# Kernel tuning notes

Measured on AMD Instinct MI355X. Metric: run time of the kernel, lower is better.

## Reference

```python
import jax, jax.numpy as jnp
import numpy as np
from jax import lax

EPS = 1e-5
TAU = 2.0
THR = 1.0

@jax.custom_vjp
def spike_fn(x):
    # torch.heaviside(x, 1.0): 1 where x >= 0, else 0
    return (x >= 0).astype(x.dtype)

def _spike_fwd(x):
    return spike_fn(x), x

def _spike_bwd(x, g):
    alpha = 4.0
    s = jax.nn.sigmoid(alpha * x)
    return (g * (1.0 - s) * s * alpha,)

spike_fn.defvjp(_spike_fwd, _spike_bwd)

def lif(x):
    # sequential membrane recurrence over dim 0 (time)
    def step(v, xt):
        v = v + (xt - v) / TAU
        s = spike_fn(v - THR)
        v = (1.0 - lax.stop_gradient(s)) * v
        return v, s
    _, spikes = lax.scan(step, jnp.zeros_like(x[0]), x)
    return spikes

def bn(x, p):
    # eval-mode BatchNorm2d; p = [weight, bias, mean, var], each [C]
    w, b, m, v = p
    inv = w / jnp.sqrt(v + EPS)
    return (x - m[None, :, None, None]) * inv[None, :, None, None] + b[None, :, None, None]

def bn_and_pad(x, p):
    # BN then pad 1 pixel on all sides with the BN-of-zero value
    w, b, m, v = p
    y = bn(x, p)
    pad_val = b - m * w / jnp.sqrt(v + EPS)  # [C]
    y = jnp.pad(y, ((0, 0), (0, 0), (1, 1), (1, 1)))
    pv = pad_val[None, :, None]  # broadcasts over batch and spatial
    y = y.at[:, :, 0, :].set(pv)
    y = y.at[:, :, -1, :].set(pv)
    y = y.at[:, :, :, 0].set(pv)
    y = y.at[:, :, :, -1].set(pv)
    return y

def branch(x, w1, dw, pw, bn3):
    # RepConv: 1x1 -> BNAndPad(1) -> depthwise3x3(valid) -> 1x1 -> BN, then outer BN
    C = x.shape[1]
    y = jnp.einsum('oc,bchw->bohw', w1, x)
    y = bn_and_pad(y, bn3[0])
    y = lax.conv_general_dilated(y, dw[:, None, :, :], (1, 1), 'VALID',
                                 dimension_numbers=('NCHW', 'OIHW', 'NCHW'),
                                 feature_group_count=C)
    y = jnp.einsum('oc,bchw->bohw', pw, y)
    y = bn(y, bn3[1])
    y = bn(y, bn3[2])
    return y

def _to_heads(t, B, N, h, d):
    # [B,C,H,W] -> [B,h,N,d]
    return t.reshape(B, h * d, N).transpose(0, 2, 1).reshape(B, N, h, d).transpose(0, 2, 1, 3)

def forward(x, q_w1, q_dw, q_pw, q_bn, k_w1, k_dw, k_pw, k_bn,
            v_w1, v_dw, v_pw, v_bn, p_w1, p_dw, p_pw, p_bn,
            num_heads=8):
    B, C, H, W = x.shape
    N = H * W
    h = num_heads
    d = C // h
    scale = float(d) ** -0.5

    xs = lif(x)
    q = lif(branch(xs, q_w1, q_dw, q_pw, q_bn))
    k = lif(branch(xs, k_w1, k_dw, k_pw, k_bn))
    v = lif(branch(xs, v_w1, v_dw, v_pw, v_bn))

    q = _to_heads(q, B, N, h, d)
    k = _to_heads(k, B, N, h, d)
    v = _to_heads(v, B, N, h, d)

    kv = jnp.einsum('bhnd,bhne->bhde', k, v)          # [B,h,d,d]
    o = jnp.einsum('bhnd,bhde->bhne', q, kv) * scale  # [B,h,N,d]
    o = o.transpose(0, 1, 3, 2).reshape(B, C, N)       # [B,C,N]
    o = lif(o)
    o = o.reshape(B, C, H, W)
    o = branch(o, p_w1, p_dw, p_pw, p_bn)
    return o.reshape(B, C, H, W)

def setup_inputs() -> dict:
    key = jax.random.key(0)
    ks = jax.random.split(key, 20)
    B, C, H, W = 8, 256, 64, 64
    s1 = 1.0 / np.sqrt(C)

    def make_bn(k):
        k1, k2, k3, k4 = jax.random.split(k, 4)
        w = 1.0 + 0.1 * jax.random.normal(k1, (3, C), jnp.float32)
        b = 0.1 * jax.random.normal(k2, (3, C), jnp.float32)
        m = 0.1 * jax.random.normal(k3, (3, C), jnp.float32)
        var = jax.random.uniform(k4, (3, C), jnp.float32, 0.5, 1.5)
        return jnp.stack([w, b, m, var], axis=1)  # [3,4,C]

    inp = {'x': jax.random.normal(ks[0], (B, C, H, W), jnp.float32)}
    for i, p in enumerate(['q', 'k', 'v', 'p']):
        kk = jax.random.split(ks[1 + i], 4)
        inp[p + '_w1'] = jax.random.normal(kk[0], (C, C), jnp.float32) * s1
        inp[p + '_dw'] = jax.random.normal(kk[1], (C, 3, 3), jnp.float32) * 0.3
        inp[p + '_pw'] = jax.random.normal(kk[2], (C, C), jnp.float32) * s1
        inp[p + '_bn'] = make_bn(kk[3])
    return inp

def reference(x, q_w1, q_dw, q_pw, q_bn, k_w1, k_dw, k_pw, k_bn,
              v_w1, v_dw, v_pw, v_bn, p_w1, p_dw, p_pw, p_bn):
    return forward(x, q_w1, q_dw, q_pw, q_bn, k_w1, k_dw, k_pw, k_bn,
                   v_w1, v_dw, v_pw, v_bn, p_w1, p_dw, p_pw, p_bn)
```

## Files before the change

kernel.cpp:

```cpp
#include <hip/hip_runtime.h>
#include <hip/hip_bf16.h>
#include <math.h>

#define T_ 8
#define C_ 256
#define N_ 4096
#define CN_ (C_ * N_)
#define EPSB 1e-5f

typedef unsigned long long u64;
typedef unsigned int u32;
typedef short bf16x8 __attribute__((ext_vector_type(8)));
typedef short bf16x4 __attribute__((ext_vector_type(4)));
typedef float f32x4 __attribute__((ext_vector_type(4)));

static __device__ __forceinline__ unsigned short f2bf(float f) {
    __hip_bfloat16 h = __float2bfloat16(f);
    return *(unsigned short*)&h;
}
static __device__ __forceinline__ float bf2f(unsigned short u) {
    u32 x = (u32)u << 16;
    return *(float*)&x;
}

typedef const __attribute__((address_space(1))) unsigned int ga_u32;
typedef __attribute__((address_space(3))) unsigned int la_u32;
static __device__ __forceinline__ void gl_lds16(const unsigned short* g,
                                                unsigned short* l_) {
    __builtin_amdgcn_global_load_lds((ga_u32*)g, (la_u32*)l_, 16, 0, 0);
}

#define DRAIN_BAR() asm volatile("s_waitcnt vmcnt(0)\ns_barrier" ::: "memory")


__global__ __launch_bounds__(256) void lif_x_frag(const float* __restrict__ X,
                                                  unsigned short* __restrict__ ST) {
    int n = blockIdx.x * 256 + threadIdx.x;
    int c0 = blockIdx.y * 8;
    int k32 = c0 >> 5, quad = (c0 >> 3) & 3;
    size_t base = (size_t)c0 * N_ + n;
    size_t pos = ((size_t)((n >> 4) * 8 + k32)) * 512 +
                 (size_t)((quad * 16 + (n & 15)) * 8);
    float v[8];
#pragma unroll
    for (int j = 0; j < 8; j++) v[j] = 0.f;
#pragma unroll
    for (int t = 0; t < T_; t++) {
        bf16x8 bs;
#pragma unroll
        for (int j = 0; j < 8; j++) {
            float xt = X[(size_t)t * CN_ + base + (size_t)j * N_];
            float vv = v[j] + (xt - v[j]) / 2.0f;
            int s = (vv - 1.0f >= 0.f) ? 1 : 0;
            bs[j] = s ? (short)0x3F80 : (short)0;
            v[j] = s ? 0.f : vv;
        }
        *(bf16x8*)&ST[(size_t)t * CN_ + pos] = bs;
    }
}

struct LArgs {
    const float* F[3];
    unsigned char* sq;
    u64* kbp;
    u64* vbp;
};
__global__ __launch_bounds__(256) void lif3(LArgs a) {
    int br = blockIdx.y;
    int idx = blockIdx.x * 256 + threadIdx.x;
    const float* X = a.F[br];
    int lane = threadIdx.x & 63;
    u64* BP = (br == 1) ? a.kbp : a.vbp;
    float v = 0.f;
#pragma unroll
    for (int t = 0; t < T_; t++) {
        float xt = X[(size_t)t * CN_ + idx];
        v = v + (xt - v) / 2.0f;
        int s = (v - 1.0f >= 0.f) ? 1 : 0;
        if (br == 0) {
            a.sq[(size_t)t * CN_ + idx] = (unsigned char)s;
        } else {
            u64 mask = __ballot(s);
            if (lane == 0) BP[((size_t)t * CN_ + idx) >> 6] = mask;
        }
        if (s) v = 0.f;
    }
}

struct WPtrs { const float* w[8]; };
__global__ __launch_bounds__(256) void split_w(WPtrs p, unsigned short* __restrict__ out) {
    int mat = blockIdx.y;
    int idx = blockIdx.x * 256 + threadIdx.x;
    int m = idx >> 8, k = idx & 255;
    float w = p.w[mat][idx];
    unsigned short h1 = f2bf(w);
    float f1 = bf2f(h1);
    unsigned short h2 = f2bf(w - f1);
    unsigned short h3 = f2bf(w - f1 - bf2f(h2));
    int lane = ((k >> 3) & 3) * 16 + (m & 15);
    size_t pos = ((size_t)(((m >> 4) * 8 + (k >> 5)) * 64 + lane)) * 8 + (k & 7);
    size_t base = (size_t)mat * 3 * 65536;
    out[base + pos] = h1;
    out[base + 65536 + pos] = h2;
    out[base + 2 * 65536 + pos] = h3;
}

static __device__ __forceinline__ void dw_body(const float* __restrict__ Yt,
                                               const float* __restrict__ dw,
                                               const float* __restrict__ bnp,
                                               unsigned short* __restrict__ Bh,
                                               unsigned short* __restrict__ Bl,
                                               int y0, int cg, int tid) {
    int c0 = cg * 8;
    __shared__ float L[8][10][68];
    __shared__ float invs[8], bs_[8], ms_[8], pads_[8];

    if (tid < 8) {
        int c = c0 + tid;
        float w = bnp[c], b = bnp[256 + c], m = bnp[512 + c], var = bnp[768 + c];
        float sq = sqrtf(var + EPSB);
        invs[tid] = w / sq;
        bs_[tid] = b;
        ms_[tid] = m;
        pads_[tid] = b - (m * w) / sq;
    }
    __syncthreads();

    for (int i = tid; i < 8 * 10 * 66; i += 256) {
        int c = i / 660;
        int rem = i - c * 660;
        int row = rem / 66, col = rem - row * 66;
        int gy = y0 - 1 + row, gx = col - 1;
        float val;
        if (gy < 0 || gy > 63 || gx < 0 || gx > 63) val = pads_[c];
        else val = (Yt[(size_t)(c0 + c) * N_ + gy * 64 + gx] - ms_[c]) * invs[c] + bs_[c];
        L[c][row][col] = val;
    }
    __syncthreads();

    int x = tid & 63, ry = tid >> 6;
#pragma unroll
    for (int h = 0; h < 2; h++) {
        int r = ry + 4 * h;
        int n = (y0 + r) * 64 + x;

        bf16x8 hi, lo;
#pragma unroll
        for (int j = 0; j < 8; j++) {
            const float* dwc = dw + (c0 + j) * 9;
            float a = 0.f;
#pragma unroll
            for (int dy = 0; dy < 3; dy++)
#pragma unroll
                for (int dx = 0; dx < 3; dx++)
                    a += dwc[dy * 3 + dx] * L[j][r + dy][x + dx];
            unsigned short hh = f2bf(a);
            hi[j] = (short)hh;
            lo[j] = (short)f2bf(a - bf2f(hh));
        }
        size_t pos = ((size_t)((n >> 4) * 8 + (cg >> 2))) * 512 +
                     (size_t)(((cg & 3) * 16 + (n & 15)) * 8);
        *(bf16x8*)&Bh[pos] = hi;
        *(bf16x8*)&Bl[pos] = lo;
    }
}

__global__ __launch_bounds__(256) void dw_bn_split(const float* __restrict__ Yin,
                                                   const float* __restrict__ dw,
                                                   const float* __restrict__ bnp,
                                                   unsigned short* __restrict__ BhT,
                                                   unsigned short* __restrict__ BlT) {
    int t = blockIdx.z;
    dw_body(Yin + (size_t)t * CN_, dw, bnp,
            BhT + (size_t)t * CN_, BlT + (size_t)t * CN_,
            blockIdx.x * 8, blockIdx.y, threadIdx.x);
}

struct DArgs {
    const float* F[3];
    const float* dw[3];
    const float* bn[3];
    unsigned short* Ph[3];
    unsigned short* Pl[3];
};
__global__ __launch_bounds__(256) void dw3(DArgs a) {
    int br = blockIdx.z >> 3, t = blockIdx.z & 7;
    dw_body(a.F[br] + (size_t)t * CN_, a.dw[br], a.bn[br],
            a.Ph[br] + (size_t)t * CN_, a.Pl[br] + (size_t)t * CN_,
            blockIdx.x * 8, blockIdx.y, threadIdx.x);
}

static __device__ __forceinline__ void gemm_s_core(const unsigned short* __restrict__ Wsp,
                                                   const unsigned short* __restrict__ Bt,
                                                   float* __restrict__ Yt,
                                                   int bx, int by, int tid) {
    int l = tid & 63, wave = tid >> 6;
    int wm = wave >> 1, wn = wave & 1;
    int lcol = l & 15, quad = l >> 4;

    __shared__ unsigned short As[2][24][512];
    __shared__ unsigned short Bs[2][8][512];

    f32x4 acc[4][4];
#pragma unroll
    for (int i = 0; i < 4; i++)
#pragma unroll
        for (int j = 0; j < 4; j++) acc[i][j] = (f32x4){0.f, 0.f, 0.f, 0.f};

    const unsigned short* src[8];
    unsigned short* d0[8];
    unsigned short* d1[8];
#pragma unroll
    for (int i = 0; i < 8; i++) {
        int tau = wave * 8 + i;
        if (tau < 24) {
            int s = tau >> 3, mtg = tau & 7;
            src[i] = &Wsp[(size_t)s * 65536 + ((size_t)((by * 8 + mtg) * 8)) * 512 + l * 8];
            d0[i] = &As[0][tau][0];
            d1[i] = &As[1][tau][0];
        } else {
            int nt = tau - 24;
            src[i] = &Bt[((size_t)((bx * 8 + nt) * 8)) * 512 + l * 8];
            d0[i] = &Bs[0][nt][0];
            d1[i] = &Bs[1][nt][0];
        }
    }

    auto stg0 = [&]() {
#pragma unroll
        for (int i = 0; i < 8; i++) { gl_lds16(src[i], d0[i]); src[i] += 512; }
    };
    auto stg1 = [&]() {
#pragma unroll
        for (int i = 0; i < 8; i++) { gl_lds16(src[i], d1[i]); src[i] += 512; }
    };
    auto compute = [&](const unsigned short (*Asp)[512],
                       const unsigned short (*Bsp)[512]) {
        bf16x8 bfr[4];
#pragma unroll
        for (int nt = 0; nt < 4; nt++)
            bfr[nt] = *(const bf16x8*)&Bsp[wn * 4 + nt][l * 8];
#pragma unroll
        for (int s = 0; s < 3; s++)
#pragma unroll
            for (int mt = 0; mt < 4; mt++) {
                bf16x8 afr = *(const bf16x8*)&Asp[s * 8 + wm * 4 + mt][l * 8];
#pragma unroll
                for (int nt = 0; nt < 4; nt++)
                    acc[mt][nt] = __builtin_amdgcn_mfma_f32_16x16x32_bf16(
                        afr, bfr[nt], acc[mt][nt], 0, 0, 0);
            }
    };

    stg0();
    DRAIN_BAR();

    for (int kk = 0; kk < 8; kk += 2) {
        stg1();
        compute(As[0], Bs[0]);
        DRAIN_BAR();
        if (kk < 6) stg0();
        compute(As[1], Bs[1]);
        DRAIN_BAR();
    }

    int m0 = by * 128, n0 = bx * 128;
#pragma unroll
    for (int mt = 0; mt < 4; mt++)
#pragma unroll
        for (int i = 0; i < 4; i++) {
            int row = m0 + wm * 64 + mt * 16 + quad * 4 + i;
            float* yr = &Yt[(size_t)row * N_ + n0 + wn * 64 + lcol];
#pragma unroll
            for (int nt = 0; nt < 4; nt++) yr[nt * 16] = acc[mt][nt][i];
        }
}

static __device__ __forceinline__ void gemm_f_core(const unsigned short* __restrict__ Wsp,
                                                   const unsigned short* __restrict__ Bht,
                                                   const unsigned short* __restrict__ Blt,
                                                   float* __restrict__ Yt,
                                                   const float* __restrict__ bnp,
                                                   int bx, int by, int tid) {
    int l = tid & 63, wave = tid >> 6;
    int wm = wave >> 1, wn = wave & 1;
    int lcol = l & 15, quad = l >> 4;

    __shared__ unsigned short As[2][24][512];
    __shared__ unsigned short Bhs[2][8][512];
    __shared__ unsigned short Bls[2][8][512];

    f32x4 acc[4][4];
#pragma unroll
    for (int i = 0; i < 4; i++)
#pragma unroll
        for (int j = 0; j < 4; j++) acc[i][j] = (f32x4){0.f, 0.f, 0.f, 0.f};

    const unsigned short* src[10];
    unsigned short* d0[10];
    unsigned short* d1[10];
#pragma unroll
    for (int i = 0; i < 10; i++) {
        int tau = wave * 10 + i;
        if (tau < 24) {
            int s = tau >> 3, mtg = tau & 7;
            src[i] = &Wsp[(size_t)s * 65536 + ((size_t)((by * 8 + mtg) * 8)) * 512 + l * 8];
            d0[i] = &As[0][tau][0];
            d1[i] = &As[1][tau][0];
        } else if (tau < 32) {
            int nt = tau - 24;
            src[i] = &Bht[((size_t)((bx * 8 + nt) * 8)) * 512 + l * 8];
            d0[i] = &Bhs[0][nt][0];
            d1[i] = &Bhs[1][nt][0];
        } else {
            int nt = tau - 32;
            src[i] = &Blt[((size_t)((bx * 8 + nt) * 8)) * 512 + l * 8];
            d0[i] = &Bls[0][nt][0];
            d1[i] = &Bls[1][nt][0];
        }
    }

    auto stg0 = [&]() {
#pragma unroll
        for (int i = 0; i < 10; i++) { gl_lds16(src[i], d0[i]); src[i] += 512; }
    };
    auto stg1 = [&]() {
#pragma unroll
        for (int i = 0; i < 10; i++) { gl_lds16(src[i], d1[i]); src[i] += 512; }
    };
    auto compute = [&](const unsigned short (*Asp)[512],
                       const unsigned short (*Bhp)[512],
                       const unsigned short (*Blp)[512]) {
        bf16x8 bh[4], bl[4];
#pragma unroll
        for (int nt = 0; nt < 4; nt++) {
            bh[nt] = *(const bf16x8*)&Bhp[wn * 4 + nt][l * 8];
            bl[nt] = *(const bf16x8*)&Blp[wn * 4 + nt][l * 8];
        }
#pragma unroll
        for (int s = 0; s < 3; s++)
#pragma unroll
            for (int mt = 0; mt < 4; mt++) {
                bf16x8 afr = *(const bf16x8*)&Asp[s * 8 + wm * 4 + mt][l * 8];
#pragma unroll
                for (int nt = 0; nt < 4; nt++)
                    acc[mt][nt] = __builtin_amdgcn_mfma_f32_16x16x32_bf16(
                        afr, bh[nt], acc[mt][nt], 0, 0, 0);
                if (s < 2) {
#pragma unroll
                    for (int nt = 0; nt < 4; nt++)
                        acc[mt][nt] = __builtin_amdgcn_mfma_f32_16x16x32_bf16(
                            afr, bl[nt], acc[mt][nt], 0, 0, 0);
                }
            }
    };

    stg0();
    DRAIN_BAR();

    for (int kk = 0; kk < 8; kk += 2) {
        stg1();
        compute(As[0], Bhs[0], Bls[0]);
        DRAIN_BAR();
        if (kk < 6) stg0();
        compute(As[1], Bhs[1], Bls[1]);
        DRAIN_BAR();
    }

    int m0 = by * 128, n0 = bx * 128;
#pragma unroll
    for (int mt = 0; mt < 4; mt++)
#pragma unroll
        for (int i = 0; i < 4; i++) {
            int row = m0 + wm * 64 + mt * 16 + quad * 4 + i;
            float i1 = bnp[1024 + row] / sqrtf(bnp[1024 + 768 + row] + EPSB);
            float b1 = bnp[1024 + 256 + row], m1 = bnp[1024 + 512 + row];
            float i2 = bnp[2048 + row] / sqrtf(bnp[2048 + 768 + row] + EPSB);
            float b2 = bnp[2048 + 256 + row], m2 = bnp[2048 + 512 + row];
            float* yr = &Yt[(size_t)row * N_ + n0 + wn * 64 + lcol];
#pragma unroll
            for (int nt = 0; nt < 4; nt++)
                yr[nt * 16] = ((acc[mt][nt][i] - m1) * i1 + b1 - m2) * i2 + b2;
        }
}

__global__ __launch_bounds__(256) void gemm_s2(const unsigned short* __restrict__ Wsp,
                                               const unsigned short* __restrict__ ST,
                                               float* __restrict__ Y) {
    int t = blockIdx.z;
    gemm_s_core(Wsp, ST + (size_t)t * CN_, Y + (size_t)t * CN_,
                blockIdx.x, blockIdx.y, threadIdx.x);
}
__global__ __launch_bounds__(256) void gemm_f2(const unsigned short* __restrict__ Wsp,
                                               const unsigned short* __restrict__ BhT,
                                               const unsigned short* __restrict__ BlT,
                                               float* __restrict__ Y,
                                               const float* __restrict__ bnp) {
    int t = blockIdx.z;
    gemm_f_core(Wsp, BhT + (size_t)t * CN_, BlT + (size_t)t * CN_,
                Y + (size_t)t * CN_, bnp, blockIdx.x, blockIdx.y, threadIdx.x);
}

struct GSArgs { const unsigned short* W[3]; const unsigned short* ST; float* F[3]; };
__global__ __launch_bounds__(256) void gemm_s3(GSArgs a) {
    int t = blockIdx.z;
    int br = blockIdx.y >> 1, byl = blockIdx.y & 1;
    gemm_s_core(a.W[br], a.ST + (size_t)t * CN_, a.F[br] + (size_t)t * CN_,
                blockIdx.x, byl, threadIdx.x);
}
struct GFArgs {
    const unsigned short* W[3];
    const unsigned short* Ph[3];
    const unsigned short* Pl[3];
    float* F[3];
    const float* bn[3];
};
__global__ __launch_bounds__(256) void gemm_f3(GFArgs a) {
    int t = blockIdx.z;
    int br = blockIdx.y >> 1, byl = blockIdx.y & 1;
    gemm_f_core(a.W[br], a.Ph[br] + (size_t)t * CN_, a.Pl[br] + (size_t)t * CN_,
                a.F[br] + (size_t)t * CN_, a.bn[br], blockIdx.x, byl, threadIdx.x);
}

__global__ __launch_bounds__(1024) void attn_kv_bp(const u64* __restrict__ Kbp,
                                                   const u64* __restrict__ Vbp,
                                                   float* __restrict__ kvbuf) {
    int th = blockIdx.x;
    int t = th >> 3, h = th & 7;
    const u64* kb = Kbp + ((size_t)t * C_ + h * 32) * 64;
    const u64* vb = Vbp + ((size_t)t * C_ + h * 32) * 64;
    __shared__ u64 ks[32][65];
    __shared__ u64 vs[32][65];
    int tid = threadIdx.x;
    {
        int r = tid >> 5, w2 = (tid & 31) * 2;
        ks[r][w2] = kb[r * 64 + w2];     ks[r][w2 + 1] = kb[r * 64 + w2 + 1];
        vs[r][w2] = vb[r * 64 + w2];     vs[r][w2 + 1] = vb[r * 64 + w2 + 1];
    }
    __syncthreads();
    int d = tid >> 5, e = tid & 31;
    int cnt = 0;
#pragma unroll
    for (int w = 0; w < 64; w++)
        cnt += __popcll(ks[d][w] & vs[e][w]);
    kvbuf[(size_t)th * 1024 + d * 32 + e] = (float)cnt;
}

__global__ __launch_bounds__(256) void attn_olif(const unsigned char* __restrict__ q,
                                                 const float* __restrict__ kvbuf,
                                                 unsigned short* __restrict__ ST) {
    int h = blockIdx.y;
    int nb = blockIdx.x * 32;
    int tid = threadIdx.x;
    int nj = tid & 31, g = tid >> 5;
    int n = nb + nj;
    int e0 = g * 4;
    __shared__ float kvs[1024];
    const float scale = 0.17677669529663687f;
    float v[4];
#pragma unroll
    for (int e = 0; e < 4; e++) v[e] = 0.f;
    size_t pos = ((size_t)((n >> 4) * 8 + h)) * 512 +
                 (size_t)(((g >> 1) * 16 + (n & 15)) * 8) + (size_t)(4 * (g & 1));
#pragma unroll
    for (int t = 0; t < T_; t++) {
        for (int i = tid; i < 1024; i += 256)
            kvs[i] = kvbuf[(size_t)(t * 8 + h) * 1024 + i];
        __syncthreads();
        float acc[4];
#pragma unroll
        for (int e = 0; e < 4; e++) acc[e] = 0.f;
        const unsigned char* qb = q + (size_t)t * CN_ + (size_t)(h * 32) * N_ + n;
#pragma unroll 4
        for (int d = 0; d < 32; d++) {
            float qd = (float)qb[(size_t)d * N_];
#pragma unroll
            for (int e = 0; e < 4; e++)
                acc[e] += qd * kvs[d * 32 + e0 + e];
        }
        bf16x4 w;
#pragma unroll
        for (int e = 0; e < 4; e++) {
            float o = acc[e] * scale;
            v[e] = v[e] + (o - v[e]) / 2.0f;
            int s = (v[e] - 1.0f >= 0.f) ? 1 : 0;
            w[e] = s ? (short)0x3F80 : (short)0;
            if (s) v[e] = 0.f;
        }
        *(bf16x4*)&ST[(size_t)t * CN_ + pos] = w;
        __syncthreads();
    }
}

extern "C" void kernel_launch(void* const* d_in, const int* in_sizes, int n_in,
                              void* d_out, int out_size, void* d_ws, size_t ws_size,
                              hipStream_t stream) {
    const float* x = (const float*)d_in[0];
    const float* q_w1 = (const float*)d_in[1];
    const float* q_dw = (const float*)d_in[2];
    const float* q_pw = (const float*)d_in[3];
    const float* q_bn = (const float*)d_in[4];
    const float* k_w1 = (const float*)d_in[5];
    const float* k_dw = (const float*)d_in[6];
    const float* k_pw = (const float*)d_in[7];
    const float* k_bn = (const float*)d_in[8];
    const float* v_w1 = (const float*)d_in[9];
    const float* v_dw = (const float*)d_in[10];
    const float* v_pw = (const float*)d_in[11];
    const float* v_bn = (const float*)d_in[12];
    const float* p_w1 = (const float*)d_in[13];
    const float* p_dw = (const float*)d_in[14];
    const float* p_pw = (const float*)d_in[15];
    const float* p_bn = (const float*)d_in[16];

    const size_t SZ = (size_t)T_ * CN_;
    float* out = (float*)d_out;
    float* F0 = (float*)d_ws;
    float* F1 = F0 + SZ;
    float* F2 = F1 + SZ;
    float* P0 = F2 + SZ;
    float* P1 = P0 + SZ;
    float* P2 = P1 + SZ;
    float* bufKV = P2 + SZ;
    unsigned char* xs = (unsigned char*)(bufKV + 65536);
    unsigned char* sq = xs + SZ;
    u64* kbp = (u64*)(sq + SZ);
    u64* vbp = kbp + (SZ >> 6);
    unsigned short* wspA = (unsigned short*)(vbp + (SZ >> 6));
    unsigned short* ST = wspA + 8 * 3 * 65536;

    unsigned short* P0h = (unsigned short*)P0; unsigned short* P0l = P0h + SZ;
    unsigned short* P1h = (unsigned short*)P1; unsigned short* P1l = P1h + SZ;
    unsigned short* P2h = (unsigned short*)P2; unsigned short* P2l = P2h + SZ;

    WPtrs wp;
    wp.w[0] = q_w1; wp.w[1] = q_pw; wp.w[2] = k_w1; wp.w[3] = k_pw;
    wp.w[4] = v_w1; wp.w[5] = v_pw; wp.w[6] = p_w1; wp.w[7] = p_pw;
    split_w<<<dim3(256, 8), dim3(256), 0, stream>>>(wp, wspA);
    const size_t WS3 = 3 * 65536;

    lif_x_frag<<<dim3(N_ / 256, C_ / 8), dim3(256), 0, stream>>>(x, ST);

    GSArgs gs;
    gs.W[0] = wspA + 0 * WS3; gs.W[1] = wspA + 2 * WS3; gs.W[2] = wspA + 4 * WS3;
    gs.ST = ST; gs.F[0] = F0; gs.F[1] = F1; gs.F[2] = F2;
    gemm_s3<<<dim3(N_ / 128, 6, T_), dim3(256), 0, stream>>>(gs);

    DArgs da;
    da.F[0] = F0; da.F[1] = F1; da.F[2] = F2;
    da.dw[0] = q_dw; da.dw[1] = k_dw; da.dw[2] = v_dw;
    da.bn[0] = q_bn; da.bn[1] = k_bn; da.bn[2] = v_bn;
    da.Ph[0] = P0h; da.Ph[1] = P1h; da.Ph[2] = P2h;
    da.Pl[0] = P0l; da.Pl[1] = P1l; da.Pl[2] = P2l;
    dw3<<<dim3(8, 32, 3 * T_), dim3(256), 0, stream>>>(da);

    GFArgs gf;
    gf.W[0] = wspA + 1 * WS3; gf.W[1] = wspA + 3 * WS3; gf.W[2] = wspA + 5 * WS3;
    gf.Ph[0] = P0h; gf.Ph[1] = P1h; gf.Ph[2] = P2h;
    gf.Pl[0] = P0l; gf.Pl[1] = P1l; gf.Pl[2] = P2l;
    gf.F[0] = F0; gf.F[1] = F1; gf.F[2] = F2;
    gf.bn[0] = q_bn; gf.bn[1] = k_bn; gf.bn[2] = v_bn;
    gemm_f3<<<dim3(N_ / 128, 6, T_), dim3(256), 0, stream>>>(gf);

    LArgs la;
    la.F[0] = F0; la.F[1] = F1; la.F[2] = F2;
    la.sq = sq; la.kbp = kbp; la.vbp = vbp;
    lif3<<<dim3(CN_ / 256, 3), dim3(256), 0, stream>>>(la);

    attn_kv_bp<<<dim3(64), dim3(1024), 0, stream>>>(kbp, vbp, bufKV);
    attn_olif<<<dim3(N_ / 32, 8), dim3(256), 0, stream>>>(sq, bufKV, ST);

    gemm_s2<<<dim3(N_ / 128, C_ / 128, T_), dim3(256), 0, stream>>>(wspA + 6 * WS3, ST, out);
    dw_bn_split<<<dim3(8, 32, T_), dim3(256), 0, stream>>>(out, p_dw, p_bn, P0h, P0l);
    gemm_f2<<<dim3(N_ / 128, C_ / 128, T_), dim3(256), 0, stream>>>(wspA + 7 * WS3, P0h, P0l, out, p_bn);
}
```

Before: 415.9 us.

## Fuse all stages into one persistent kernel with software grid barriers

Replaces the eleven separate kernel launches with a single persistent kernel of 512 blocks. It walks through each stage's virtual block indices and separates the stages with an atomic-counter grid barrier. Shared memory is unified through a union, and the KV popcount stage is split across four blocks per head. The goal is to remove per-launch overhead and launch gaps between stages. In exchange it caps concurrency at 512 resident blocks, and it depends on every block being co-resident, otherwise the barrier deadlocks. The shared union is sized by the largest stage, which may reduce occupancy.

```diff
diff --git a/kernel.cpp b/kernel.cpp
--- a/kernel.cpp
+++ b/kernel.cpp
@@ -7,6 +7,7 @@
 #define N_ 4096
 #define CN_ (C_ * N_)
 #define EPSB 1e-5f
+#define NBLK 512
 
 typedef unsigned long long u64;
 typedef unsigned int u32;
@@ -32,11 +33,39 @@
 
 #define DRAIN_BAR() asm volatile("s_waitcnt vmcnt(0)\ns_barrier" ::: "memory")
 
-
-__global__ __launch_bounds__(256) void lif_x_frag(const float* __restrict__ X,
-                                                  unsigned short* __restrict__ ST) {
-    int n = blockIdx.x * 256 + threadIdx.x;
-    int c0 = blockIdx.y * 8;
+union SharedU {
+    struct { unsigned short As[2][24][512]; unsigned short Bs[2][8][512]; } s;
+    struct { unsigned short As[2][24][512]; unsigned short Bh[2][8][512];
+             unsigned short Bl[2][8][512]; } f;
+    struct { float L[8][10][68]; float invs[8], bs[8], ms[8], pads[8]; } dw;
+    struct { u64 ks[8][65]; u64 vs[32][65]; } kv;
+    float kvs[1024];
+};
+
+static __device__ __forceinline__ void grid_barrier(unsigned* bar) {
+    __syncthreads();
+    if (threadIdx.x == 0) {
+        __threadfence();
+        unsigned g = __hip_atomic_load(&bar[1], __ATOMIC_RELAXED, __HIP_MEMORY_SCOPE_AGENT);
+        unsigned a = __hip_atomic_fetch_add(&bar[0], 1u, __ATOMIC_ACQ_REL, __HIP_MEMORY_SCOPE_AGENT);
+        if (a == NBLK - 1u) {
+            __hip_atomic_store(&bar[0], 0u, __ATOMIC_RELAXED, __HIP_MEMORY_SCOPE_AGENT);
+            __hip_atomic_fetch_add(&bar[1], 1u, __ATOMIC_RELEASE, __HIP_MEMORY_SCOPE_AGENT);
+        } else {
+            while (__hip_atomic_load(&bar[1], __ATOMIC_RELAXED, __HIP_MEMORY_SCOPE_AGENT) == g)
+                __builtin_amdgcn_s_sleep(2);
+        }
+        __threadfence();
+    }
+    __syncthreads();
+}
+
+
+static __device__ __forceinline__ void lifx_body(const float* __restrict__ X,
+                                                 unsigned short* __restrict__ ST,
+                                                 int bx, int by, int tid) {
+    int n = bx * 256 + tid;
+    int c0 = by * 8;
     int k32 = c0 >> 5, quad = (c0 >> 3) & 3;
     size_t base = (size_t)c0 * N_ + n;
     size_t pos = ((size_t)((n >> 4) * 8 + k32)) * 512 +
@@ -59,44 +88,15 @@
     }
 }
 
-struct LArgs {
-    const float* F[3];
-    unsigned char* sq;
-    u64* kbp;
-    u64* vbp;
-};
-__global__ __launch_bounds__(256) void lif3(LArgs a) {
-    int br = blockIdx.y;
-    int idx = blockIdx.x * 256 + threadIdx.x;
-    const float* X = a.F[br];
-    int lane = threadIdx.x & 63;
-    u64* BP = (br == 1) ? a.kbp : a.vbp;
-    float v = 0.f;
-#pragma unroll
-    for (int t = 0; t < T_; t++) {
-        float xt = X[(size_t)t * CN_ + idx];
-        v = v + (xt - v) / 2.0f;
-        int s = (v - 1.0f >= 0.f) ? 1 : 0;
-        if (br == 0) {
-            a.sq[(size_t)t * CN_ + idx] = (unsigned char)s;
-        } else {
-            u64 mask = __ballot(s);
-            if (lane == 0) BP[((size_t)t * CN_ + idx) >> 6] = mask;
-        }
-        if (s) v = 0.f;
-    }
-}
-
-struct WPtrs { const float* w[8]; };
-__global__ __launch_bounds__(256) void split_w(WPtrs p, unsigned short* __restrict__ out) {
-    int mat = blockIdx.y;
-    int idx = blockIdx.x * 256 + threadIdx.x;
+static __device__ __forceinline__ void splitw_body(const float* __restrict__ w,
+                                                   unsigned short* __restrict__ out,
+                                                   int mat, int idx) {
     int m = idx >> 8, k = idx & 255;
-    float w = p.w[mat][idx];
-    unsigned short h1 = f2bf(w);
+    float wv = w[idx];
+    unsigned short h1 = f2bf(wv);
     float f1 = bf2f(h1);
-    unsigned short h2 = f2bf(w - f1);
-    unsigned short h3 = f2bf(w - f1 - bf2f(h2));
+    unsigned short h2 = f2bf(wv - f1);
+    unsigned short h3 = f2bf(wv - f1 - bf2f(h2));
     int lane = ((k >> 3) & 3) * 16 + (m & 15);
     size_t pos = ((size_t)(((m >> 4) * 8 + (k >> 5)) * 64 + lane)) * 8 + (k & 7);
     size_t base = (size_t)mat * 3 * 65536;
@@ -110,10 +110,13 @@
                                                const float* __restrict__ bnp,
                                                unsigned short* __restrict__ Bh,
                                                unsigned short* __restrict__ Bl,
-                                               int y0, int cg, int tid) {
+                                               int y0, int cg, int tid, SharedU* sh) {
     int c0 = cg * 8;
-    __shared__ float L[8][10][68];
-    __shared__ float invs[8], bs_[8], ms_[8], pads_[8];
+    float (*L)[10][68] = sh->dw.L;
+    float* invs = sh->dw.invs;
+    float* bs_ = sh->dw.bs;
+    float* ms_ = sh->dw.ms;
+    float* pads_ = sh->dw.pads;
 
     if (tid < 8) {
         int c = c0 + tid;
@@ -143,7 +146,6 @@
     for (int h = 0; h < 2; h++) {
         int r = ry + 4 * h;
         int n = (y0 + r) * 64 + x;
-
         bf16x8 hi, lo;
 #pragma unroll
         for (int j = 0; j < 8; j++) {
@@ -163,43 +165,18 @@
         *(bf16x8*)&Bh[pos] = hi;
         *(bf16x8*)&Bl[pos] = lo;
     }
-}
-
-__global__ __launch_bounds__(256) void dw_bn_split(const float* __restrict__ Yin,
-                                                   const float* __restrict__ dw,
-                                                   const float* __restrict__ bnp,
-                                                   unsigned short* __restrict__ BhT,
-                                                   unsigned short* __restrict__ BlT) {
-    int t = blockIdx.z;
-    dw_body(Yin + (size_t)t * CN_, dw, bnp,
-            BhT + (size_t)t * CN_, BlT + (size_t)t * CN_,
-            blockIdx.x * 8, blockIdx.y, threadIdx.x);
-}
-
-struct DArgs {
-    const float* F[3];
-    const float* dw[3];
-    const float* bn[3];
-    unsigned short* Ph[3];
-    unsigned short* Pl[3];
-};
-__global__ __launch_bounds__(256) void dw3(DArgs a) {
-    int br = blockIdx.z >> 3, t = blockIdx.z & 7;
-    dw_body(a.F[br] + (size_t)t * CN_, a.dw[br], a.bn[br],
-            a.Ph[br] + (size_t)t * CN_, a.Pl[br] + (size_t)t * CN_,
-            blockIdx.x * 8, blockIdx.y, threadIdx.x);
+    __syncthreads();
 }
 
 static __device__ __forceinline__ void gemm_s_core(const unsigned short* __restrict__ Wsp,
                                                    const unsigned short* __restrict__ Bt,
                                                    float* __restrict__ Yt,
-                                                   int bx, int by, int tid) {
+                                                   int bx, int by, int tid,
+                                                   unsigned short (*As)[24][512],
+                                                   unsigned short (*Bs)[8][512]) {
     int l = tid & 63, wave = tid >> 6;
     int wm = wave >> 1, wn = wave & 1;
     int lcol = l & 15, quad = l >> 4;
-
-    __shared__ unsigned short As[2][24][512];
-    __shared__ unsigned short Bs[2][8][512];
 
     f32x4 acc[4][4];
 #pragma unroll
@@ -254,7 +231,6 @@
 
     stg0();
     DRAIN_BAR();
-
     for (int kk = 0; kk < 8; kk += 2) {
         stg1();
         compute(As[0], Bs[0]);
@@ -281,14 +257,13 @@
                                                    const unsigned short* __restrict__ Blt,
                                                    float* __restrict__ Yt,
                                                    const float* __restrict__ bnp,
-                                                   int bx, int by, int tid) {
+                                                   int bx, int by, int tid,
+                                                   unsigned short (*As)[24][512],
+                                                   unsigned short (*Bhs)[8][512],
+                                                   unsigned short (*Bls)[8][512]) {
     int l = tid & 63, wave = tid >> 6;
     int wm = wave >> 1, wn = wave & 1;
     int lcol = l & 15, quad = l >> 4;
-
-    __shared__ unsigned short As[2][24][512];
-    __shared__ unsigned short Bhs[2][8][512];
-    __shared__ unsigned short Bls[2][8][512];
 
     f32x4 acc[4][4];
 #pragma unroll
@@ -357,7 +332,6 @@
 
     stg0();
     DRAIN_BAR();
-
     for (int kk = 0; kk < 8; kk += 2) {
         stg1();
         compute(As[0], Bhs[0], Bls[0]);
@@ -384,78 +358,60 @@
         }
 }
 
-__global__ __launch_bounds__(256) void gemm_s2(const unsigned short* __restrict__ Wsp,
-                                               const unsigned short* __restrict__ ST,
-                                               float* __restrict__ Y) {
-    int t = blockIdx.z;
-    gemm_s_core(Wsp, ST + (size_t)t * CN_, Y + (size_t)t * CN_,
-                blockIdx.x, blockIdx.y, threadIdx.x);
-}
-__global__ __launch_bounds__(256) void gemm_f2(const unsigned short* __restrict__ Wsp,
-                                               const unsigned short* __restrict__ BhT,
-                                               const unsigned short* __restrict__ BlT,
-                                               float* __restrict__ Y,
-                                               const float* __restrict__ bnp) {
-    int t = blockIdx.z;
-    gemm_f_core(Wsp, BhT + (size_t)t * CN_, BlT + (size_t)t * CN_,
-                Y + (size_t)t * CN_, bnp, blockIdx.x, blockIdx.y, threadIdx.x);
-}
-
-struct GSArgs { const unsigned short* W[3]; const unsigned short* ST; float* F[3]; };
-__global__ __launch_bounds__(256) void gemm_s3(GSArgs a) {
-    int t = blockIdx.z;
-    int br = blockIdx.y >> 1, byl = blockIdx.y & 1;
-    gemm_s_core(a.W[br], a.ST + (size_t)t * CN_, a.F[br] + (size_t)t * CN_,
-                blockIdx.x, byl, threadIdx.x);
-}
-struct GFArgs {
-    const unsigned short* W[3];
-    const unsigned short* Ph[3];
-    const unsigned short* Pl[3];
-    float* F[3];
-    const float* bn[3];
-};
-__global__ __launch_bounds__(256) void gemm_f3(GFArgs a) {
-    int t = blockIdx.z;
-    int br = blockIdx.y >> 1, byl = blockIdx.y & 1;
-    gemm_f_core(a.W[br], a.Ph[br] + (size_t)t * CN_, a.Pl[br] + (size_t)t * CN_,
-                a.F[br] + (size_t)t * CN_, a.bn[br], blockIdx.x, byl, threadIdx.x);
-}
-
-__global__ __launch_bounds__(1024) void attn_kv_bp(const u64* __restrict__ Kbp,
-                                                   const u64* __restrict__ Vbp,
-                                                   float* __restrict__ kvbuf) {
-    int th = blockIdx.x;
-    int t = th >> 3, h = th & 7;
-    const u64* kb = Kbp + ((size_t)t * C_ + h * 32) * 64;
-    const u64* vb = Vbp + ((size_t)t * C_ + h * 32) * 64;
-    __shared__ u64 ks[32][65];
-    __shared__ u64 vs[32][65];
-    int tid = threadIdx.x;
-    {
-        int r = tid >> 5, w2 = (tid & 31) * 2;
-        ks[r][w2] = kb[r * 64 + w2];     ks[r][w2 + 1] = kb[r * 64 + w2 + 1];
-        vs[r][w2] = vb[r * 64 + w2];     vs[r][w2 + 1] = vb[r * 64 + w2 + 1];
+static __device__ __forceinline__ void lif3_body(const float* __restrict__ X,
+                                                 unsigned char* sq, u64* kbp, u64* vbp,
+                                                 int br, int idx, int tid) {
+    int lane = tid & 63;
+    u64* BP = (br == 1) ? kbp : vbp;
+    float v = 0.f;
+#pragma unroll
+    for (int t = 0; t < T_; t++) {
+        float xt = X[(size_t)t * CN_ + idx];
+        v = v + (xt - v) / 2.0f;
+        int s = (v - 1.0f >= 0.f) ? 1 : 0;
+        if (br == 0) {
+            sq[(size_t)t * CN_ + idx] = (unsigned char)s;
+        } else {
+            u64 mask = __ballot(s);
+            if (lane == 0) BP[((size_t)t * CN_ + idx) >> 6] = mask;
+        }
+        if (s) v = 0.f;
+    }
+}
+
+static __device__ __forceinline__ void kv_body(const u64* __restrict__ kb,
+                                               const u64* __restrict__ vb_,
+                                               float* __restrict__ kvout,
+                                               int q, int tid, SharedU* sh) {
+    u64 (*ks)[65] = sh->kv.ks;
+    u64 (*vs)[65] = sh->kv.vs;
+    for (int i = tid; i < 512; i += 256) {
+        int r = i >> 6, w = i & 63;
+        ks[r][w] = kb[(q * 8 + r) * 64 + w];
+    }
+    for (int i = tid; i < 2048; i += 256) {
+        int r = i >> 6, w = i & 63;
+        vs[r][w] = vb_[r * 64 + w];
     }
     __syncthreads();
-    int d = tid >> 5, e = tid & 31;
+    int dq = tid >> 5, e = tid & 31;
     int cnt = 0;
 #pragma unroll
     for (int w = 0; w < 64; w++)
-        cnt += __popcll(ks[d][w] & vs[e][w]);
-    kvbuf[(size_t)th * 1024 + d * 32 + e] = (float)cnt;
-}
-
-__global__ __launch_bounds__(256) void attn_olif(const unsigned char* __restrict__ q,
+        cnt += __popcll(ks[dq][w] & vs[e][w]);
+    kvout[(q * 8 + dq) * 32 + e] = (float)cnt;
+    __syncthreads();
+}
+
+static __device__ __forceinline__ void olif_body(const unsigned char* __restrict__ q,
                                                  const float* __restrict__ kvbuf,
-                                                 unsigned short* __restrict__ ST) {
-    int h = blockIdx.y;
-    int nb = blockIdx.x * 32;
-    int tid = threadIdx.x;
+                                                 unsigned short* __restrict__ ST,
+                                                 int bx, int h, int tid, SharedU* sh) {
+    float* kvs = sh->kvs;
+    int nb = bx * 32;
     int nj = tid & 31, g = tid >> 5;
     int n = nb + nj;
     int e0 = g * 4;
-    __shared__ float kvs[1024];
     const float scale = 0.17677669529663687f;
     float v[4];
 #pragma unroll
@@ -489,6 +445,117 @@
         }
         *(bf16x4*)&ST[(size_t)t * CN_ + pos] = w;
         __syncthreads();
+    }
+}
+
+struct MegaArgs {
+    const float* x;
+    const float* w8[8];
+    const float* dwp[3];
+    const float* bnp[3];
+    const float* p_dw;
+    const float* p_bn;
+    unsigned short* wspA;
+    unsigned short* ST;
+    float* F[3];
+    unsigned short* Ph[3];
+    unsigned short* Pl[3];
+    unsigned char* sq;
+    u64* kbp;
+    u64* vbp;
+    float* kvbuf;
+    float* out;
+    unsigned short* Pph;
+    unsigned short* Ppl;
+    unsigned* bar;
+};
+
+__global__ __launch_bounds__(256, 2) void mega(MegaArgs a) {
+    __shared__ SharedU sh;
+    int bid = blockIdx.x, tid = threadIdx.x;
+    const size_t WS3 = 3 * 65536;
+
+    for (int vb = bid; vb < 2560; vb += NBLK) {
+        if (vb < 2048) splitw_body(a.w8[vb >> 8], a.wspA, vb >> 8, (vb & 255) * 256 + tid);
+        else { int u = vb - 2048; lifx_body(a.x, a.ST, u & 15, u >> 4, tid); }
+    }
+    grid_barrier(a.bar);
+
+    for (int r = 0; r < 3; r++) {
+        int vb = bid + r * NBLK;
+        int bx = vb & 31, rest = vb >> 5;
+        int y = rest % 6, t = rest / 6;
+        int br = y >> 1, byl = y & 1;
+        gemm_s_core(a.wspA + (size_t)(br * 2) * WS3, a.ST + (size_t)t * CN_,
+                    a.F[br] + (size_t)t * CN_, bx, byl, tid, sh.s.As, sh.s.Bs);
+    }
+    grid_barrier(a.bar);
+
+    for (int r = 0; r < 12; r++) {
+        int vb = bid + r * NBLK;
+        int x8 = vb & 7, y = (vb >> 3) & 31, z = vb >> 8;
+        int br = z >> 3, t = z & 7;
+        dw_body(a.F[br] + (size_t)t * CN_, a.dwp[br], a.bnp[br],
+                a.Ph[br] + (size_t)t * CN_, a.Pl[br] + (size_t)t * CN_,
+                x8 * 8, y, tid, &sh);
+    }
+    grid_barrier(a.bar);
+
+    for (int r = 0; r < 3; r++) {
+        int vb = bid + r * NBLK;
+        int bx = vb & 31, rest = vb >> 5;
+        int y = rest % 6, t = rest / 6;
+        int br = y >> 1, byl = y & 1;
+        gemm_f_core(a.wspA + (size_t)(br * 2 + 1) * WS3,
+                    a.Ph[br] + (size_t)t * CN_, a.Pl[br] + (size_t)t * CN_,
+                    a.F[br] + (size_t)t * CN_, a.bnp[br], bx, byl, tid,
+                    sh.f.As, sh.f.Bh, sh.f.Bl);
+    }
+    grid_barrier(a.bar);
+
+    for (int r = 0; r < 24; r++) {
+        int vb = bid + r * NBLK;
+        int blk = vb & 4095, br = vb >> 12;
+        lif3_body(a.F[br], a.sq, a.kbp, a.vbp, br, blk * 256 + tid, tid);
+    }
+    grid_barrier(a.bar);
+
+    if (bid < 256) {
+        int th = bid >> 2, q = bid & 3;
+        int t = th >> 3, h = th & 7;
+        kv_body(a.kbp + ((size_t)t * C_ + h * 32) * 64,
+                a.vbp + ((size_t)t * C_ + h * 32) * 64,
+                a.kvbuf + (size_t)th * 1024, q, tid, &sh);
+    }
+    grid_barrier(a.bar);
+
+    for (int r = 0; r < 2; r++) {
+        int vb = bid + r * NBLK;
+        olif_body(a.sq, a.kvbuf, a.ST, vb & 127, vb >> 7, tid, &sh);
+    }
+    grid_barrier(a.bar);
+
+    {
+        int bx = bid & 31, by = (bid >> 5) & 1, t = bid >> 6;
+        gemm_s_core(a.wspA + 6 * WS3, a.ST + (size_t)t * CN_,
+                    a.out + (size_t)t * CN_, bx, by, tid, sh.s.As, sh.s.Bs);
+    }
+    grid_barrier(a.bar);
+
+    for (int r = 0; r < 4; r++) {
+        int vb = bid + r * NBLK;
+        int x8 = vb & 7, y = (vb >> 3) & 31, t = vb >> 8;
+        dw_body(a.out + (size_t)t * CN_, a.p_dw, a.p_bn,
+                a.Pph + (size_t)t * CN_, a.Ppl + (size_t)t * CN_,
+                x8 * 8, y, tid, &sh);
+    }
+    grid_barrier(a.bar);
+
+    {
+        int bx = bid & 31, by = (bid >> 5) & 1, t = bid >> 6;
+        gemm_f_core(a.wspA + 7 * WS3, a.Pph + (size_t)t * CN_, a.Ppl + (size_t)t * CN_,
+                    a.out + (size_t)t * CN_, a.p_bn, bx, by, tid,
+                    sh.f.As, sh.f.Bh, sh.f.Bl);
     }
 }
 
@@ -533,44 +600,24 @@
     unsigned short* P1h = (unsigned short*)P1; unsigned short* P1l = P1h + SZ;
     unsigned short* P2h = (unsigned short*)P2; unsigned short* P2l = P2h + SZ;
 
-    WPtrs wp;
-    wp.w[0] = q_w1; wp.w[1] = q_pw; wp.w[2] = k_w1; wp.w[3] = k_pw;
-    wp.w[4] = v_w1; wp.w[5] = v_pw; wp.w[6] = p_w1; wp.w[7] = p_pw;
-    split_w<<<dim3(256, 8), dim3(256), 0, stream>>>(wp, wspA);
-    const size_t WS3 = 3 * 65536;
-
-    lif_x_frag<<<dim3(N_ / 256, C_ / 8), dim3(256), 0, stream>>>(x, ST);
-
-    GSArgs gs;
-    gs.W[0] = wspA + 0 * WS3; gs.W[1] = wspA + 2 * WS3; gs.W[2] = wspA + 4 * WS3;
-    gs.ST = ST; gs.F[0] = F0; gs.F[1] = F1; gs.F[2] = F2;
-    gemm_s3<<<dim3(N_ / 128, 6, T_), dim3(256), 0, stream>>>(gs);
-
-    DArgs da;
-    da.F[0] = F0; da.F[1] = F1; da.F[2] = F2;
-    da.dw[0] = q_dw; da.dw[1] = k_dw; da.dw[2] = v_dw;
-    da.bn[0] = q_bn; da.bn[1] = k_bn; da.bn[2] = v_bn;
-    da.Ph[0] = P0h; da.Ph[1] = P1h; da.Ph[2] = P2h;
-    da.Pl[0] = P0l; da.Pl[1] = P1l; da.Pl[2] = P2l;
-    dw3<<<dim3(8, 32, 3 * T_), dim3(256), 0, stream>>>(da);
-
-    GFArgs gf;
-    gf.W[0] = wspA + 1 * WS3; gf.W[1] = wspA + 3 * WS3; gf.W[2] = wspA + 5 * WS3;
-    gf.Ph[0] = P0h; gf.Ph[1] = P1h; gf.Ph[2] = P2h;
-    gf.Pl[0] = P0l; gf.Pl[1] = P1l; gf.Pl[2] = P2l;
-    gf.F[0] = F0; gf.F[1] = F1; gf.F[2] = F2;
-    gf.bn[0] = q_bn; gf.bn[1] = k_bn; gf.bn[2] = v_bn;
-    gemm_f3<<<dim3(N_ / 128, 6, T_), dim3(256), 0, stream>>>(gf);
-
-    LArgs la;
-    la.F[0] = F0; la.F[1] = F1; la.F[2] = F2;
-    la.sq = sq; la.kbp = kbp; la.vbp = vbp;
-    lif3<<<dim3(CN_ / 256, 3), dim3(256), 0, stream>>>(la);
-
-    attn_kv_bp<<<dim3(64), dim3(1024), 0, stream>>>(kbp, vbp, bufKV);
-    attn_olif<<<dim3(N_ / 32, 8), dim3(256), 0, stream>>>(sq, bufKV, ST);
-
-    gemm_s2<<<dim3(N_ / 128, C_ / 128, T_), dim3(256), 0, stream>>>(wspA + 6 * WS3, ST, out);
-    dw_bn_split<<<dim3(8, 32, T_), dim3(256), 0, stream>>>(out, p_dw, p_bn, P0h, P0l);
-    gemm_f2<<<dim3(N_ / 128, C_ / 128, T_), dim3(256), 0, stream>>>(wspA + 7 * WS3, P0h, P0l, out, p_bn);
-}
+    unsigned* bar = (unsigned*)xs;
+    hipMemsetAsync(bar, 0, 16, stream);
+
+    MegaArgs ma;
+    ma.x = x;
+    ma.w8[0] = q_w1; ma.w8[1] = q_pw; ma.w8[2] = k_w1; ma.w8[3] = k_pw;
+    ma.w8[4] = v_w1; ma.w8[5] = v_pw; ma.w8[6] = p_w1; ma.w8[7] = p_pw;
+    ma.dwp[0] = q_dw; ma.dwp[1] = k_dw; ma.dwp[2] = v_dw;
+    ma.bnp[0] = q_bn; ma.bnp[1] = k_bn; ma.bnp[2] = v_bn;
+    ma.p_dw = p_dw; ma.p_bn = p_bn;
+    ma.wspA = wspA; ma.ST = ST;
+    ma.F[0] = F0; ma.F[1] = F1; ma.F[2] = F2;
+    ma.Ph[0] = P0h; ma.Ph[1] = P1h; ma.Ph[2] = P2h;
+    ma.Pl[0] = P0l; ma.Pl[1] = P1l; ma.Pl[2] = P2l;
+    ma.sq = sq; ma.kbp = kbp; ma.vbp = vbp; ma.kvbuf = bufKV;
+    ma.out = out;
+    ma.Pph = P0h; ma.Ppl = P0l;
+    ma.bar = bar;
+
+    mega<<<dim3(NBLK), dim3(256), 0, stream>>>(ma);
+}
```

Result: slower. 1.206 ms (+190.0%).
